# Performance work log

Hardware: AMD Instinct MI355X
Metric: run time of the kernel (lower is better)

Reference implementation:

```python
import jax, jax.numpy as jnp
import numpy as np


def setup_inputs() -> dict:
    key = jax.random.key(0)
    ks = jax.random.split(key, 6)
    B, L, H = 32, 2048, 1024
    return {
        "hidden_state": jax.random.normal(ks[0], (B, H), dtype=jnp.float32),
        "encoder_outputs": jax.random.normal(ks[1], (L, B, 2 * H), dtype=jnp.float32),
        "reduce_W": jax.random.normal(ks[2], (H, 2 * H), dtype=jnp.float32) * 0.02,
        "reduce_b": jax.random.normal(ks[3], (H,), dtype=jnp.float32) * 0.02,
        "attn_W": jax.random.normal(ks[4], (H, H), dtype=jnp.float32) * 0.02,
        "attn_b": jax.random.normal(ks[5], (H,), dtype=jnp.float32) * 0.02,
    }


def reference(hidden_state, encoder_outputs, reduce_W, reduce_b, attn_W, attn_b):
    # reduce_linear: [L, B, 2H] -> [L, B, H]
    reduced = jnp.einsum("lbk,hk->lbh", encoder_outputs, reduce_W) + reduce_b
    # 'general' score: dot(hidden_state[b], attn_linear(reduced[l, b]))
    proj = jnp.einsum("lbh,gh->lbg", reduced, attn_W) + attn_b  # [L, B, H]
    scores = jnp.einsum("bh,lbh->bl", hidden_state, proj)  # [B, L]
    return jax.nn.softmax(scores, axis=1)
```

## Files before the change

kernel.cpp:

```cpp
#include <hip/hip_runtime.h>

#define B 32
#define L 2048
#define H 1024
#define K2 2048
#define NL 8
#define HSPLIT 16
#define HCHUNK (H / HSPLIT)

__global__ __launch_bounds__(256) void v_kernel(const float* __restrict__ hs,
                                                const float* __restrict__ attn_W,
                                                float* __restrict__ v) {
    int tid = blockIdx.x * 256 + threadIdx.x;
    int b = tid >> 10;
    int h = tid & (H - 1);
    const float* hsb = hs + b * H;
    float acc = 0.f;
    #pragma unroll 8
    for (int g = 0; g < H; ++g)
        acc = fmaf(hsb[g], attn_W[g * H + h], acc);
    v[tid] = acc;
}

__global__ __launch_bounds__(256) void w_partial_kernel(const float* __restrict__ v,
                                                        const float* __restrict__ rW,
                                                        float* __restrict__ pw) {
    int k2 = blockIdx.x * 256 + threadIdx.x;
    int h0 = blockIdx.y * HCHUNK;
    const float2* rW2 = (const float2*)rW;
    float2 acc[B];
    #pragma unroll
    for (int b = 0; b < B; ++b) { acc[b].x = 0.f; acc[b].y = 0.f; }
    for (int h = h0; h < h0 + HCHUNK; ++h) {
        float2 rw = rW2[h * (K2 / 2) + k2];
        #pragma unroll
        for (int b = 0; b < B; ++b) {
            float vb = v[b * H + h];
            acc[b].x = fmaf(vb, rw.x, acc[b].x);
            acc[b].y = fmaf(vb, rw.y, acc[b].y);
        }
    }
    float2* pw2 = (float2*)pw;
    #pragma unroll
    for (int b = 0; b < B; ++b)
        pw2[(blockIdx.y * B + b) * (K2 / 2) + k2] = acc[b];
}

__global__ __launch_bounds__(256) void w_reduce_kernel(const float* __restrict__ pw,
                                                       float* __restrict__ w) {
    int i = blockIdx.x * 256 + threadIdx.x;
    float s = 0.f;
    #pragma unroll
    for (int p = 0; p < HSPLIT; ++p) s += pw[p * (B * K2) + i];
    w[i] = s;
}

__global__ __launch_bounds__(256) void scores_kernel(const float4* __restrict__ enc,
                                                     const float4* __restrict__ w,
                                                     float* __restrict__ scores) {
    int wid  = blockIdx.x * 4 + (threadIdx.x >> 6);
    int lane = threadIdx.x & 63;
    int b  = wid & (B - 1);
    int l0 = (wid >> 5) * NL;
    const float4* wb = w + b * (K2 / 4);
    float acc[NL];
    #pragma unroll
    for (int i = 0; i < NL; ++i) acc[i] = 0.f;
    for (int j = 0; j < (K2 / 4) / 64; ++j) {
        int idx = j * 64 + lane;
        float4 wv = wb[idx];
        #pragma unroll
        for (int i = 0; i < NL; ++i) {
            float4 e = enc[(size_t)((l0 + i) * B + b) * (K2 / 4) + idx];
            acc[i] = fmaf(wv.x, e.x, acc[i]);
            acc[i] = fmaf(wv.y, e.y, acc[i]);
            acc[i] = fmaf(wv.z, e.z, acc[i]);
            acc[i] = fmaf(wv.w, e.w, acc[i]);
        }
    }
    #pragma unroll
    for (int i = 0; i < NL; ++i) {
        float s = acc[i];
        #pragma unroll
        for (int off = 32; off > 0; off >>= 1) s += __shfl_down(s, off, 64);
        if (lane == 0) scores[b * L + l0 + i] = s;
    }
}

__global__ __launch_bounds__(256) void softmax_kernel(float* __restrict__ out) {
    int b = blockIdx.x;
    int t = threadIdx.x;
    float* row = out + b * L;
    float vals[8];
    float m = -3.4e38f;
    #pragma unroll
    for (int i = 0; i < 8; ++i) { vals[i] = row[t + i * 256]; m = fmaxf(m, vals[i]); }
    __shared__ float wred[4];
    int wv = t >> 6, lane = t & 63;
    #pragma unroll
    for (int off = 1; off < 64; off <<= 1) m = fmaxf(m, __shfl_xor(m, off, 64));
    if (lane == 0) wred[wv] = m;
    __syncthreads();
    m = fmaxf(fmaxf(wred[0], wred[1]), fmaxf(wred[2], wred[3]));
    __syncthreads();
    float s = 0.f;
    #pragma unroll
    for (int i = 0; i < 8; ++i) { vals[i] = __expf(vals[i] - m); s += vals[i]; }
    #pragma unroll
    for (int off = 1; off < 64; off <<= 1) s += __shfl_xor(s, off, 64);
    if (lane == 0) wred[wv] = s;
    __syncthreads();
    s = wred[0] + wred[1] + wred[2] + wred[3];
    float inv = 1.f / s;
    #pragma unroll
    for (int i = 0; i < 8; ++i) row[t + i * 256] = vals[i] * inv;
}

extern "C" void kernel_launch(void* const* d_in, const int* in_sizes, int n_in,
                              void* d_out, int out_size, void* d_ws, size_t ws_size,
                              hipStream_t stream) {
    const float* hs  = (const float*)d_in[0];
    const float* enc = (const float*)d_in[1];
    const float* rW  = (const float*)d_in[2];
    const float* aW  = (const float*)d_in[4];
    float* out = (float*)d_out;

    char* ws = (char*)d_ws;
    float* v  = (float*)(ws);
    float* w  = (float*)(ws + 131072);
    float* pw = (float*)(ws + 131072 + 262144);

    v_kernel<<<(B * H) / 256, 256, 0, stream>>>(hs, aW, v);

    dim3 g2(K2 / 512, HSPLIT);
    w_partial_kernel<<<g2, 256, 0, stream>>>(v, rW, pw);
    w_reduce_kernel<<<(B * K2) / 256, 256, 0, stream>>>(pw, w);

    scores_kernel<<<(L / NL) * B / 4, 256, 0, stream>>>((const float4*)enc,
                                                        (const float4*)w, out);
    softmax_kernel<<<B, 256, 0, stream>>>(out);
}
```

Before: 816.8 us.

## Stream encoder rows with nontemporal loads, cache w in registers, split accumulators

The scores kernel now preloads the per-batch w vector into registers and walks each encoder row in turn, using nontemporal loads and four independent accumulators. The v kernel also gets split accumulators to break the FMA dependency chain, and HSPLIT doubles to give the w partial kernel more blocks. The aim is better memory-level parallelism on the dominant 512MB encoder read and less cache pollution. In exchange, the w reduce step has twice as many partials to sum and register pressure rises.

```diff
diff --git a/kernel.cpp b/kernel.cpp
--- a/kernel.cpp
+++ b/kernel.cpp
@@ -5,8 +5,10 @@
 #define H 1024
 #define K2 2048
 #define NL 8
-#define HSPLIT 16
+#define HSPLIT 32
 #define HCHUNK (H / HSPLIT)
+
+typedef float f4 __attribute__((ext_vector_type(4)));
 
 __global__ __launch_bounds__(256) void v_kernel(const float* __restrict__ hs,
                                                 const float* __restrict__ attn_W,
@@ -15,11 +17,15 @@
     int b = tid >> 10;
     int h = tid & (H - 1);
     const float* hsb = hs + b * H;
-    float acc = 0.f;
-    #pragma unroll 8
-    for (int g = 0; g < H; ++g)
-        acc = fmaf(hsb[g], attn_W[g * H + h], acc);
-    v[tid] = acc;
+    float a0 = 0.f, a1 = 0.f, a2 = 0.f, a3 = 0.f;
+    #pragma unroll 4
+    for (int g = 0; g < H; g += 4) {
+        a0 = fmaf(hsb[g + 0], attn_W[(g + 0) * H + h], a0);
+        a1 = fmaf(hsb[g + 1], attn_W[(g + 1) * H + h], a1);
+        a2 = fmaf(hsb[g + 2], attn_W[(g + 2) * H + h], a2);
+        a3 = fmaf(hsb[g + 3], attn_W[(g + 3) * H + h], a3);
+    }
+    v[tid] = (a0 + a1) + (a2 + a3);
 }
 
 __global__ __launch_bounds__(256) void w_partial_kernel(const float* __restrict__ v,
@@ -55,28 +61,36 @@
     w[i] = s;
 }
 
-__global__ __launch_bounds__(256) void scores_kernel(const float4* __restrict__ enc,
-                                                     const float4* __restrict__ w,
+__global__ __launch_bounds__(256) void scores_kernel(const f4* __restrict__ enc,
+                                                     const f4* __restrict__ w,
                                                      float* __restrict__ scores) {
     int wid  = blockIdx.x * 4 + (threadIdx.x >> 6);
     int lane = threadIdx.x & 63;
     int b  = wid & (B - 1);
     int l0 = (wid >> 5) * NL;
-    const float4* wb = w + b * (K2 / 4);
+    const f4* wb = w + b * (K2 / 4) + lane;
+    f4 wr[8];
+    #pragma unroll
+    for (int j = 0; j < 8; ++j) wr[j] = wb[j * 64];
     float acc[NL];
-    #pragma unroll
-    for (int i = 0; i < NL; ++i) acc[i] = 0.f;
-    for (int j = 0; j < (K2 / 4) / 64; ++j) {
-        int idx = j * 64 + lane;
-        float4 wv = wb[idx];
+    #pragma unroll 2
+    for (int i = 0; i < NL; ++i) {
+        const f4* row = enc + ((size_t)(l0 + i) * B + b) * (K2 / 4) + lane;
+        float a0 = 0.f, a1 = 0.f, a2 = 0.f, a3 = 0.f;
         #pragma unroll
-        for (int i = 0; i < NL; ++i) {
-            float4 e = enc[(size_t)((l0 + i) * B + b) * (K2 / 4) + idx];
-            acc[i] = fmaf(wv.x, e.x, acc[i]);
-            acc[i] = fmaf(wv.y, e.y, acc[i]);
-            acc[i] = fmaf(wv.z, e.z, acc[i]);
-            acc[i] = fmaf(wv.w, e.w, acc[i]);
+        for (int j = 0; j < 8; j += 2) {
+            f4 ea = __builtin_nontemporal_load(row + (j + 0) * 64);
+            f4 eb = __builtin_nontemporal_load(row + (j + 1) * 64);
+            a0 = fmaf(wr[j].x, ea.x, a0);
+            a1 = fmaf(wr[j].y, ea.y, a1);
+            a2 = fmaf(wr[j].z, ea.z, a2);
+            a3 = fmaf(wr[j].w, ea.w, a3);
+            a0 = fmaf(wr[j + 1].x, eb.x, a0);
+            a1 = fmaf(wr[j + 1].y, eb.y, a1);
+            a2 = fmaf(wr[j + 1].z, eb.z, a2);
+            a3 = fmaf(wr[j + 1].w, eb.w, a3);
         }
+        acc[i] = (a0 + a1) + (a2 + a3);
     }
     #pragma unroll
     for (int i = 0; i < NL; ++i) {
@@ -136,7 +150,7 @@
     w_partial_kernel<<<g2, 256, 0, stream>>>(v, rW, pw);
     w_reduce_kernel<<<(B * K2) / 256, 256, 0, stream>>>(pw, w);
 
-    scores_kernel<<<(L / NL) * B / 4, 256, 0, stream>>>((const float4*)enc,
-                                                        (const float4*)w, out);
+    scores_kernel<<<(L / NL) * B / 4, 256, 0, stream>>>((const f4*)enc,
+                                                        (const f4*)w, out);
     softmax_kernel<<<B, 256, 0, stream>>>(out);
 }
```

New measurement: 741.3 us. -9.2%, faster.
